# Performance work log

Hardware: AMD Instinct MI355X
Metric: run time of the kernel (lower is better)

## Reference

```python
import jax, jax.numpy as jnp
import numpy as np

N_NODES = 20000
N_EDGES = 100000
ATOM_F = 40
BOND_F = 10
H = 32          # n_node_hidden
EH = 128        # n_edge_hidden
N_LAYERS = 3
EPS = 1e-5
NEG_SLOPE = 0.8


def _bn(x, g, b):
    # BatchNorm1d in training mode: batch mean / biased variance over dim 0
    m = x.mean(0)
    v = x.var(0)
    return (x - m) * jax.lax.rsqrt(v + EPS) * g + b


def setup_inputs() -> dict:
    key = jax.random.key(0)
    ks = iter(jax.random.split(key, 32))

    def nrm(shape, scale):
        return jax.random.normal(next(ks), shape, dtype=jnp.float32) * scale

    inp = {
        "x_node": jax.random.normal(next(ks), (N_NODES, ATOM_F), dtype=jnp.float32),
        "x_edge": jax.random.normal(next(ks), (N_EDGES, BOND_F), dtype=jnp.float32),
        "src": jax.random.randint(next(ks), (N_EDGES,), 0, N_NODES, dtype=jnp.int32),
        "dst": jax.random.randint(next(ks), (N_EDGES,), 0, N_NODES, dtype=jnp.int32),
        # Embedding params
        "bn_n_g": jnp.ones((ATOM_F,), jnp.float32),
        "bn_n_b": jnp.zeros((ATOM_F,), jnp.float32),
        "node_W": nrm((ATOM_F, H), 1.0 / np.sqrt(ATOM_F)),
        "node_b": jnp.zeros((H,), jnp.float32),
        "bn_e_g": jnp.ones((BOND_F,), jnp.float32),
        "bn_e_b": jnp.zeros((BOND_F,), jnp.float32),
        "edge_W": nrm((BOND_F, EH), 1.0 / np.sqrt(BOND_F)),
        "edge_b": jnp.zeros((EH,), jnp.float32),
        # Edge-network (NNConv edge_func) params
        "en_W1": nrm((EH, EH), 1.0 / np.sqrt(EH)),
        "en_b1": jnp.zeros((EH,), jnp.float32),
        "en_bn1_g": jnp.ones((EH,), jnp.float32),
        "en_bn1_b": jnp.zeros((EH,), jnp.float32),
        "en_W2": nrm((EH, H * H), 1.0 / np.sqrt(EH)),
        "en_b2": jnp.zeros((H * H,), jnp.float32),
        "en_bn2_g": jnp.ones((H * H,), jnp.float32),
        "en_bn2_b": jnp.zeros((H * H,), jnp.float32),
        # GRU params (torch layout: [3H, in], gate order r,z,n)
        "gru_Wih": nrm((3 * H, H), 1.0 / np.sqrt(H)),
        "gru_Whh": nrm((3 * H, H), 1.0 / np.sqrt(H)),
        "gru_bih": jnp.zeros((3 * H,), jnp.float32),
        "gru_bhh": jnp.zeros((3 * H,), jnp.float32),
    }
    return inp


def reference(x_node, x_edge, src, dst,
              bn_n_g, bn_n_b, node_W, node_b,
              bn_e_g, bn_e_b, edge_W, edge_b,
              en_W1, en_b1, en_bn1_g, en_bn1_b,
              en_W2, en_b2, en_bn2_g, en_bn2_b,
              gru_Wih, gru_Whh, gru_bih, gru_bhh):
    # ---- Embedding ----
    h_node = _bn(x_node, bn_n_g, bn_n_b) @ node_W + node_b          # [N, H]
    h_edge = _bn(x_edge, bn_e_g, bn_e_b) @ edge_W + edge_b          # [E, EH]

    # ---- Edge network (depends only on h_edge; identical every layer) ----
    t = _bn(h_edge @ en_W1 + en_b1, en_bn1_g, en_bn1_b)
    t = jnp.where(t > 0, t, NEG_SLOPE * t)                          # LeakyReLU(0.8)
    W_e = _bn(t @ en_W2 + en_b2, en_bn2_g, en_bn2_b).reshape(-1, H, H)  # [E, H, H]

    # mean-aggregation denominator (zero in-degree -> message stays 0)
    deg = jax.ops.segment_sum(jnp.ones_like(dst, jnp.float32), dst, num_segments=N_NODES)
    denom = jnp.maximum(deg, 1.0)[:, None]                          # [N, 1]

    def gru_cell(x, h):
        gi = x @ gru_Wih.T + gru_bih
        gh = h @ gru_Whh.T + gru_bhh
        gi_r, gi_z, gi_n = jnp.split(gi, 3, axis=-1)
        gh_r, gh_z, gh_n = jnp.split(gh, 3, axis=-1)
        r = jax.nn.sigmoid(gi_r + gh_r)
        z = jax.nn.sigmoid(gi_z + gh_z)
        n = jnp.tanh(gi_n + r * gh_n)
        return (1.0 - z) * n + z * h

    h = h_node
    for _ in range(N_LAYERS):
        msg = jnp.einsum('ei,eio->eo', h[src], W_e)                 # per-edge matmul
        m = jax.ops.segment_sum(msg, dst, num_segments=N_NODES) / denom  # scatter-mean
        h = gru_cell(m, h)
    return h
```

## Files before the change

kernel.cpp:

```cpp
#include <hip/hip_runtime.h>
#include <hip/hip_fp16.h>

#define NN 20000
#define NE 100000
#define TSQ_NB 256

typedef _Float16 f16x8 __attribute__((ext_vector_type(8)));
typedef float f32x4 __attribute__((ext_vector_type(4)));

__device__ __forceinline__ float wred(float v) {
#pragma unroll
  for (int k = 1; k < 64; k <<= 1) v += __shfl_xor(v, k);
  return v;
}

__global__ __launch_bounds__(256) void pre0(float* __restrict__ zbase,
                                            const float* __restrict__ edge_W,
                                            const float* __restrict__ edge_b,
                                            const float* __restrict__ en_W1,
                                            const float* __restrict__ en_b1,
                                            float* __restrict__ Wc, float* __restrict__ bc) {
  int bid = blockIdx.x, t = threadIdx.x;
  if (bid < 145) {
    int i = bid * 256 + t;
    if (i < 36896) zbase[i] = 0.f;
  } else {
    for (int idx = t; idx < 1280; idx += 256) {
      int bq = idx >> 7, j = idx & 127;
      float a = 0.f;
      for (int q = 0; q < 128; ++q) a += edge_W[bq * 128 + q] * en_W1[q * 128 + j];
      Wc[idx] = a;
    }
    if (t < 128) {
      float a = en_b1[t];
      for (int q = 0; q < 128; ++q) a += edge_b[q] * en_W1[q * 128 + t];
      bc[t] = a;
    }
  }
}

__global__ __launch_bounds__(256) void pre1(const float* __restrict__ x_node,
                                            const float* __restrict__ x_edge,
                                            const int* __restrict__ dst,
                                            float* __restrict__ nstat,
                                            float* __restrict__ estat,
                                            float* __restrict__ deg) {
  __shared__ float ls40[80];
  __shared__ float ls10[20];
  int bid = blockIdx.x, t = threadIdx.x;
  if (bid < 200) {
    for (int i = t; i < 80; i += 256) ls40[i] = 0.f;
    __syncthreads();
    for (int idx = bid * 256 + t; idx < NN * 40; idx += 200 * 256) {
      float v = x_node[idx];
      int c = idx % 40;
      atomicAdd(&ls40[c], v);
      atomicAdd(&ls40[40 + c], v * v);
    }
    __syncthreads();
    for (int i = t; i < 80; i += 256) atomicAdd(&nstat[i], ls40[i]);
  } else if (bid < 456) {
    int b2 = bid - 200;
    for (int i = t; i < 20; i += 256) ls10[i] = 0.f;
    __syncthreads();
    for (int idx = b2 * 256 + t; idx < NE * 10; idx += 256 * 256) {
      float v = x_edge[idx];
      int c = idx % 10;
      atomicAdd(&ls10[c], v);
      atomicAdd(&ls10[10 + c], v * v);
    }
    __syncthreads();
    for (int i = t; i < 20; i += 256) atomicAdd(&estat[i], ls10[i]);
  } else {
    int e = (bid - 456) * 256 + t;
    if (e < NE) atomicAdd(&deg[dst[e]], 1.f);
  }
}

__global__ __launch_bounds__(256) void pre2(const float* __restrict__ nstat,
                                            const float* __restrict__ estat,
                                            const float* __restrict__ bn_n_g,
                                            const float* __restrict__ bn_n_b,
                                            const float* __restrict__ bn_e_g,
                                            const float* __restrict__ bn_e_b,
                                            const float* __restrict__ deg,
                                            float* __restrict__ ns, float* __restrict__ nc,
                                            float* __restrict__ es, float* __restrict__ ec,
                                            float* __restrict__ inv_den) {
  int bid = blockIdx.x, t = threadIdx.x;
  if (bid == 0) {
    if (t < 40) {
      float invR = 1.f / (float)NN;
      float mean = nstat[t] * invR;
      float var = fmaxf(nstat[40 + t] * invR - mean * mean, 0.f);
      float sc = bn_n_g[t] * rsqrtf(var + 1e-5f);
      ns[t] = sc;
      nc[t] = bn_n_b[t] - mean * sc;
    }
  } else if (bid == 1) {
    if (t < 10) {
      float invR = 1.f / (float)NE;
      float mean = estat[t] * invR;
      float var = fmaxf(estat[10 + t] * invR - mean * mean, 0.f);
      float sc = bn_e_g[t] * rsqrtf(var + 1e-5f);
      es[t] = sc;
      ec[t] = bn_e_b[t] - mean * sc;
    }
  } else {
    int n = (bid - 2) * 256 + t;
    if (n < NN) inv_den[n] = 1.f / fmaxf(deg[n], 1.f);
  }
}

__global__ __launch_bounds__(256) void pre3(const float* __restrict__ x_edge,
                                            const float* __restrict__ es,
                                            const float* __restrict__ ec,
                                            float* __restrict__ sxs,
                                            const float* __restrict__ x_node,
                                            const float* __restrict__ ns,
                                            const float* __restrict__ nc,
                                            const float* __restrict__ node_W,
                                            const float* __restrict__ node_b,
                                            float* __restrict__ h_out) {
  __shared__ float Wl[40 * 32];
  __shared__ float sl[40], cl[40];
  int bid = blockIdx.x, t = threadIdx.x;
  if (bid < 32) {
    float s[10][10], xs[10], esl[10], ecl[10];
#pragma unroll
    for (int a = 0; a < 10; ++a) {
      xs[a] = 0.f; esl[a] = es[a]; ecl[a] = ec[a];
#pragma unroll
      for (int b = 0; b < 10; ++b) s[a][b] = 0.f;
    }
    for (int e = bid * 256 + t; e < NE; e += 32 * 256) {
      float xb[10];
#pragma unroll
      for (int q = 0; q < 10; ++q) xb[q] = x_edge[(size_t)e * 10 + q] * esl[q] + ecl[q];
#pragma unroll
      for (int a = 0; a < 10; ++a) {
        xs[a] += xb[a];
#pragma unroll
        for (int b = 0; b < 10; ++b) s[a][b] += xb[a] * xb[b];
      }
    }
#pragma unroll
    for (int a = 0; a < 10; ++a) {
      float r = wred(xs[a]);
      if ((t & 63) == 0) atomicAdd(&sxs[100 + a], r);
#pragma unroll
      for (int b = 0; b < 10; ++b) {
        float r2 = wred(s[a][b]);
        if ((t & 63) == 0) atomicAdd(&sxs[a * 10 + b], r2);
      }
    }
  } else {
    for (int i = t; i < 1280; i += 256) Wl[i] = node_W[i];
    if (t < 40) { sl[t] = ns[t]; cl[t] = nc[t]; }
    __syncthreads();
    int gid = (bid - 32) * 256 + t;
    if (gid >= NN * 32) return;
    int r = gid >> 5, j = gid & 31;
    float acc = node_b[j];
#pragma unroll
    for (int k = 0; k < 40; ++k)
      acc += (x_node[(size_t)r * 40 + k] * sl[k] + cl[k]) * Wl[k * 32 + j];
    h_out[gid] = acc;
  }
}

__global__ void bn1_from_sx(const float* __restrict__ sxs, const float* __restrict__ Wc,
                            const float* __restrict__ bc, const float* __restrict__ g,
                            const float* __restrict__ b, float* __restrict__ s1,
                            float* __restrict__ c1) {
  int j = threadIdx.x;
  float w[10];
#pragma unroll
  for (int q = 0; q < 10; ++q) w[q] = Wc[q * 128 + j];
  float d = 0.f;
#pragma unroll
  for (int q = 0; q < 10; ++q) d += sxs[100 + q] * w[q];
  float qq = 0.f;
#pragma unroll
  for (int a = 0; a < 10; ++a) {
    float p = 0.f;
#pragma unroll
    for (int bq = 0; bq < 10; ++bq) p += sxs[a * 10 + bq] * w[bq];
    qq += w[a] * p;
  }
  float invE = 1.f / (float)NE;
  float bias = bc[j];
  float mean = d * invE + bias;
  float m2 = (qq + 2.f * bias * d) * invE + bias * bias;
  float var = fmaxf(m2 - mean * mean, 0.f);
  float sc = g[j] * rsqrtf(var + 1e-5f);
  s1[j] = sc;
  c1[j] = b[j] - mean * sc;
}

__global__ __launch_bounds__(256) void t_kernel(const float* __restrict__ x,
                                                const float* __restrict__ es,
                                                const float* __restrict__ ec,
                                                const float* __restrict__ Wc,
                                                const float* __restrict__ bcb,
                                                const float* __restrict__ s1,
                                                const float* __restrict__ c1,
                                                __half* __restrict__ T, int E) {
  __shared__ float Wcl[1280], bcl[128], s1l[128], c1l[128], esl[10], ecl[10];
  __shared__ float xr[16][10];
  int t = threadIdx.x;
  for (int i = t; i < 1280; i += 256) Wcl[i] = Wc[i];
  if (t < 128) { bcl[t] = bcb[t]; s1l[t] = s1[t]; c1l[t] = c1[t]; }
  if (t < 10) { esl[t] = es[t]; ecl[t] = ec[t]; }
  int r0 = blockIdx.x * 16;
  if (t < 160) xr[t / 10][t % 10] = x[(size_t)r0 * 10 + t];
  __syncthreads();
  int rl = t >> 4, c0 = (t & 15) * 8;
  float acc[8];
#pragma unroll
  for (int j = 0; j < 8; ++j) acc[j] = bcl[c0 + j];
#pragma unroll
  for (int q = 0; q < 10; ++q) {
    float xb = xr[rl][q] * esl[q] + ecl[q];
#pragma unroll
    for (int j = 0; j < 8; ++j) acc[j] += xb * Wcl[q * 128 + c0 + j];
  }
  f16x8 o;
#pragma unroll
  for (int j = 0; j < 8; ++j) {
    float tv = acc[j] * s1l[c0 + j] + c1l[c0 + j];
    tv = tv > 0.f ? tv : 0.8f * tv;
    o[j] = (_Float16)tv;
  }
  *(f16x8*)&T[(size_t)(r0 + rl) * 128 + c0] = o;
}

__global__ __launch_bounds__(256) void pre6(const __half* __restrict__ T,
                                            float* __restrict__ tsum,
                                            float* __restrict__ partial, int E) {
  __shared__ float cs[128];
  __shared__ _Float16 tl[32 * 132];
  int bid = blockIdx.x, t = threadIdx.x;
  if (bid < 512) {
    int col = t & 127, hf = t >> 7;
    float a = 0.f;
    for (int r = bid * 2 + hf; r < E; r += 512 * 2)
      a += __half2float(T[(size_t)r * 128 + col]);
    if (hf) cs[col] = a;
    __syncthreads();
    if (!hf) atomicAdd(&tsum[col], a + cs[col]);
  } else {
    int bq = bid - 512;
    int w = t >> 6, lane = t & 63;
    int g = lane >> 4, cl = lane & 15;
    f32x4 acc[2][8];
#pragma unroll
    for (int i = 0; i < 2; ++i)
#pragma unroll
      for (int j = 0; j < 8; ++j) acc[i][j] = {0.f, 0.f, 0.f, 0.f};
    int nch = E >> 5;
    for (int ch = bq; ch < nch; ch += TSQ_NB) {
      __syncthreads();
#pragma unroll
      for (int p = 0; p < 4; ++p) {
        int u = p * 256 + t;
        int e = u >> 5, c0 = (u & 31) * 4;
        *(uint2*)&tl[e * 132 + c0] = *(const uint2*)&T[((size_t)ch * 32 + e) * 128 + c0];
      }
      __syncthreads();
      f16x8 fr[8];
#pragma unroll
      for (int cb = 0; cb < 8; ++cb) {
        f16x8 f;
#pragma unroll
        for (int j = 0; j < 8; ++j) f[j] = tl[(g * 8 + j) * 132 + cb * 16 + cl];
        fr[cb] = f;
      }
      f16x8 afr[2];
#pragma unroll
      for (int ri = 0; ri < 2; ++ri) {
        int cb = w * 2 + ri;
        f16x8 f;
#pragma unroll
        for (int j = 0; j < 8; ++j) f[j] = tl[(g * 8 + j) * 132 + cb * 16 + cl];
        afr[ri] = f;
      }
#pragma unroll
      for (int ri = 0; ri < 2; ++ri)
#pragma unroll
        for (int ci = 0; ci < 8; ++ci)
          acc[ri][ci] = __builtin_amdgcn_mfma_f32_16x16x32_f16(afr[ri], fr[ci], acc[ri][ci], 0, 0, 0);
    }
    float* pb = partial + (size_t)bq * 16384;
#pragma unroll
    for (int ri = 0; ri < 2; ++ri)
#pragma unroll
      for (int ci = 0; ci < 8; ++ci)
#pragma unroll
        for (int q = 0; q < 4; ++q)
          pb[(w * 32 + ri * 16 + g * 4 + q) * 128 + ci * 16 + cl] = acc[ri][ci][q];
  }
}

__global__ void tsq_reduce(const float* __restrict__ partial, float* __restrict__ S) {
  int i = blockIdx.x * 256 + threadIdx.x;
  float a = 0.f;
  for (int b = 0; b < TSQ_NB; ++b) a += partial[(size_t)b * 16384 + i];
  S[i] = a;
}

__global__ __launch_bounds__(256) void bn2p(const float* __restrict__ S,
                                            const float* __restrict__ tsum,
                                            const float* __restrict__ W2,
                                            const float* __restrict__ b2,
                                            const float* __restrict__ g,
                                            const float* __restrict__ b,
                                            float* __restrict__ s2, float* __restrict__ c2p) {
  __shared__ float Sl[16384];
  __shared__ float tsl[128];
  for (int i = threadIdx.x; i < 16384; i += 256) Sl[i] = S[i];
  if (threadIdx.x < 128) tsl[threadIdx.x] = tsum[threadIdx.x];
  __syncthreads();
  int w = threadIdx.x >> 6, lane = threadIdx.x & 63;
  int io = blockIdx.x * 4 + w;
  float wlo = W2[(size_t)lane * 1024 + io];
  float whi = W2[(size_t)(lane + 64) * 1024 + io];
  float plo = 0.f, phi = 0.f;
#pragma unroll
  for (int a = 0; a < 64; ++a) {
    float wa = __shfl(wlo, a);
    plo += wa * Sl[a * 128 + lane];
    phi += wa * Sl[a * 128 + lane + 64];
  }
#pragma unroll
  for (int a = 0; a < 64; ++a) {
    float wa = __shfl(whi, a);
    plo += wa * Sl[(a + 64) * 128 + lane];
    phi += wa * Sl[(a + 64) * 128 + lane + 64];
  }
  float qq = wred(plo * wlo + phi * whi);
  float d = wred(wlo * tsl[lane] + whi * tsl[lane + 64]);
  if (lane == 0) {
    float invE = 1.f / (float)NE;
    float mean_raw = d * invE;
    float var = fmaxf(qq * invE - mean_raw * mean_raw, 0.f);
    float sc = g[io] * rsqrtf(var + 1e-5f);
    s2[io] = sc;
    c2p[io] = b[io] - (mean_raw + b2[io]) * sc;
  }
}

__global__ __launch_bounds__(256) void pre9(const float* __restrict__ W2,
                                            const float* __restrict__ s2,
                                            unsigned short* __restrict__ Bp,
                                            const float* __restrict__ h,
                                            const float* __restrict__ c2p,
                                            float* __restrict__ hc,
                                            float* __restrict__ m) {
  __shared__ float cl[1024];
  int bid = blockIdx.x, t = threadIdx.x;
  if (bid < 64) {
    int idx = bid * 256 + t;
    int cb = idx >> 8;
    int ks = (idx >> 6) & 3;
    int lane = idx & 63;
    int col = cb * 16 + (lane & 15);
    int kbase = ks * 32 + (lane >> 4) * 8;
    float sc = s2[col];
    unsigned short tmp[8];
#pragma unroll
    for (int j = 0; j < 8; ++j)
      tmp[j] = __half_as_ushort(__float2half(W2[(size_t)(kbase + j) * 1024 + col] * sc));
    *(uint4*)&Bp[(size_t)idx * 8] = *(uint4*)tmp;
  } else {
    for (int i = t; i < 1024; i += 256) cl[i] = c2p[i];
    __syncthreads();
    int gid = (bid - 64) * 256 + t;
    if (gid >= NN * 32) return;
    int n = gid >> 5, o = gid & 31;
    float a = 0.f;
#pragma unroll
    for (int i = 0; i < 32; ++i) a += h[(size_t)n * 32 + i] * cl[i * 32 + o];
    hc[gid] = a;
    m[gid] = 0.f;
  }
}

__global__ __launch_bounds__(256, 3) void msg_mfma(const __half* __restrict__ T,
                                                   const unsigned short* __restrict__ Bp,
                                                   const float* __restrict__ h,
                                                   const float* __restrict__ hc,
                                                   const int* __restrict__ src,
                                                   const int* __restrict__ dst,
                                                   float* __restrict__ m, int E) {
  __shared__ float hst[32 * 36];
  __shared__ float msw[4 * 1056];
  int t = threadIdx.x;
  int w = t >> 6, lane = t & 63;
  int arow = lane & 15, kgrp = lane >> 4;
  int e0 = blockIdx.x * 32;
  {
    int row = t >> 3, i0 = (t & 7) * 4;
    int sn = src[e0 + row];
    float4 hv = *(const float4*)&h[(size_t)sn * 32 + i0];
    hst[(i0 + 0) * 36 + row] = hv.x;
    hst[(i0 + 1) * 36 + row] = hv.y;
    hst[(i0 + 2) * 36 + row] = hv.z;
    hst[(i0 + 3) * 36 + row] = hv.w;
  }
  __syncthreads();
  f16x8 ah[4][2];
#pragma unroll
  for (int ks = 0; ks < 4; ++ks)
#pragma unroll
    for (int ri = 0; ri < 2; ++ri)
      ah[ks][ri] = *(const f16x8*)&T[(size_t)(e0 + ri * 16 + arow) * 128 + ks * 32 + kgrp * 8];
  f32x4 pm[2][2];
#pragma unroll
  for (int p = 0; p < 2; ++p)
#pragma unroll
    for (int ri = 0; ri < 2; ++ri) pm[p][ri] = {0.f, 0.f, 0.f, 0.f};
#pragma unroll
  for (int cb = 0; cb < 4; ++cb) {
    f32x4 acc[2][4];
#pragma unroll
    for (int i = 0; i < 2; ++i)
#pragma unroll
      for (int j = 0; j < 4; ++j) acc[i][j] = {0.f, 0.f, 0.f, 0.f};
#pragma unroll
    for (int ks = 0; ks < 4; ++ks) {
#pragma unroll
      for (int ci = 0; ci < 4; ++ci) {
        int f = cb * 16 + w * 4 + ci;
        f16x8 bv = *(const f16x8*)&Bp[((size_t)(f * 4 + ks) * 64 + lane) * 8];
        acc[0][ci] = __builtin_amdgcn_mfma_f32_16x16x32_f16(ah[ks][0], bv, acc[0][ci], 0, 0, 0);
        acc[1][ci] = __builtin_amdgcn_mfma_f32_16x16x32_f16(ah[ks][1], bv, acc[1][ci], 0, 0, 0);
      }
    }
#pragma unroll
    for (int ci = 0; ci < 4; ++ci) {
      int i = cb * 8 + w * 2 + (ci >> 1);
#pragma unroll
      for (int ri = 0; ri < 2; ++ri) {
        f32x4 hv = *(const f32x4*)&hst[i * 36 + ri * 16 + kgrp * 4];
        if (ci & 1) pm[1][ri] += hv * acc[ri][ci];
        else        pm[0][ri] += hv * acc[ri][ci];
      }
    }
  }
  {
    float* mw = &msw[w * 1056];
#pragma unroll
    for (int p = 0; p < 2; ++p) {
      int o = p * 16 + arow;
#pragma unroll
      for (int ri = 0; ri < 2; ++ri) {
        int rb = ri * 16 + kgrp * 4;
        mw[o * 33 + rb + 0] = pm[p][ri][0];
        mw[o * 33 + rb + 1] = pm[p][ri][1];
        mw[o * 33 + rb + 2] = pm[p][ri][2];
        mw[o * 33 + rb + 3] = pm[p][ri][3];
      }
    }
  }
  __syncthreads();
  {
    int row = t >> 3, o0 = (t & 7) * 4;
    int e = e0 + row;
    int sn = src[e], dn = dst[e];
    float* mp = m + (size_t)dn * 32;
    const float* hcp = hc + (size_t)sn * 32;
#pragma unroll
    for (int j = 0; j < 4; ++j) {
      int o = o0 + j;
      float v = msw[0 * 1056 + o * 33 + row] + msw[1 * 1056 + o * 33 + row] +
                msw[2 * 1056 + o * 33 + row] + msw[3 * 1056 + o * 33 + row];
      v += hcp[o];
      atomicAdd(&mp[o], v);
    }
  }
}

__global__ __launch_bounds__(256) void gru_kernel(const float* __restrict__ m,
                                                  const float* __restrict__ inv_den,
                                                  const float* __restrict__ h_in,
                                                  const float* __restrict__ Wih,
                                                  const float* __restrict__ Whh,
                                                  const float* __restrict__ bih,
                                                  const float* __restrict__ bhh,
                                                  float* __restrict__ h_out,
                                                  const float* __restrict__ c2p,
                                                  float* __restrict__ hc_out,
                                                  float* __restrict__ m_next,
                                                  int do_next, int N) {
  __shared__ float WT[32 * 96], UT[32 * 96];
  __shared__ float c2l[1024];
  __shared__ float hnew[256];
  int t = threadIdx.x;
  for (int idx = t; idx < 96 * 32; idx += 256) {
    int j = idx / 32, i = idx % 32;
    WT[i * 96 + j] = Wih[idx];
    UT[i * 96 + j] = Whh[idx];
  }
  if (do_next)
    for (int i = t; i < 1024; i += 256) c2l[i] = c2p[i];
  __syncthreads();
  int gid = blockIdx.x * 256 + t;
  int n = gid >> 5, o = gid & 31;
  float inv = inv_den[n];
  float air = 0.f, aiz = 0.f, ain = 0.f, ahr = 0.f, ahz = 0.f, ahn = 0.f;
#pragma unroll
  for (int i = 0; i < 32; ++i) {
    float mi = m[(size_t)n * 32 + i] * inv;
    float hi = h_in[(size_t)n * 32 + i];
    const float* w = &WT[i * 96 + o];
    const float* u = &UT[i * 96 + o];
    air += mi * w[0];  aiz += mi * w[32];  ain += mi * w[64];
    ahr += hi * u[0];  ahz += hi * u[32];  ahn += hi * u[64];
  }
  float r = 1.f / (1.f + expf(-(air + bih[o] + ahr + bhh[o])));
  float z = 1.f / (1.f + expf(-(aiz + bih[o + 32] + ahz + bhh[o + 32])));
  float ng = tanhf(ain + bih[o + 64] + r * (ahn + bhh[o + 64]));
  float hval = (1.f - z) * ng + z * h_in[(size_t)n * 32 + o];
  h_out[gid] = hval;
  if (do_next) {
    hnew[t] = hval;
    __syncthreads();
    int nl = t >> 5;
    float a = 0.f;
#pragma unroll
    for (int i = 0; i < 32; ++i) a += hnew[nl * 32 + i] * c2l[i * 32 + o];
    hc_out[gid] = a;
    m_next[gid] = 0.f;
  }
}

extern "C" void kernel_launch(void* const* d_in, const int* in_sizes, int n_in,
                              void* d_out, int out_size, void* d_ws, size_t ws_size,
                              hipStream_t stream) {
  const float* x_node = (const float*)d_in[0];
  const float* x_edge = (const float*)d_in[1];
  const int* src = (const int*)d_in[2];
  const int* dst = (const int*)d_in[3];
  const float* bn_n_g = (const float*)d_in[4];
  const float* bn_n_b = (const float*)d_in[5];
  const float* node_W = (const float*)d_in[6];
  const float* node_b = (const float*)d_in[7];
  const float* bn_e_g = (const float*)d_in[8];
  const float* bn_e_b = (const float*)d_in[9];
  const float* edge_W = (const float*)d_in[10];
  const float* edge_b = (const float*)d_in[11];
  const float* en_W1 = (const float*)d_in[12];
  const float* en_b1 = (const float*)d_in[13];
  const float* en_W2 = (const float*)d_in[16];
  const float* en_b2 = (const float*)d_in[17];
  const float* en_bn2_g = (const float*)d_in[18];
  const float* en_bn2_b = (const float*)d_in[19];
  const float* en_bn1_g = (const float*)d_in[14];
  const float* en_bn1_b = (const float*)d_in[15];
  const float* gWih = (const float*)d_in[20];
  const float* gWhh = (const float*)d_in[21];
  const float* gbih = (const float*)d_in[22];
  const float* gbhh = (const float*)d_in[23];
  float* out = (float*)d_out;

  char* ws = (char*)d_ws;
  __half* Tt      = (__half*)(ws + 0);
  float* tsq_part = (float*)(ws + 25600000);
  float* h_a      = (float*)(ws + 42377216);
  float* h_b      = (float*)(ws + 44937216);
  float* m_buf    = (float*)(ws + 47497216);
  float* hc       = (float*)(ws + 50057216);
  float* inv_den  = (float*)(ws + 52617216);
  float* zbase    = (float*)(ws + 52697216);
  float* deg   = zbase;
  float* S     = zbase + 20000;
  float* tsum  = zbase + 36384;
  float* sxs   = zbase + 36512;
  float* nstat = zbase + 36640;
  float* estat = zbase + 36768;
  float* par   = (float*)(ws + 52844800);
  float* ns = par + 0;    float* nc = par + 64;
  float* es = par + 128;  float* ec = par + 192;
  float* s1 = par + 256;  float* c1 = par + 384;
  float* wc = par + 512;
  float* bcb = par + 1792;
  float* s2 = par + 1920; float* c2p = par + 2944;
  unsigned short* Bp = (unsigned short*)(ws + 52861184);

  pre0<<<146, 256, 0, stream>>>(zbase, edge_W, edge_b, en_W1, en_b1, wc, bcb);
  pre1<<<847, 256, 0, stream>>>(x_node, x_edge, dst, nstat, estat, deg);
  pre2<<<81, 256, 0, stream>>>(nstat, estat, bn_n_g, bn_n_b, bn_e_g, bn_e_b, deg,
                               ns, nc, es, ec, inv_den);
  pre3<<<2532, 256, 0, stream>>>(x_edge, es, ec, sxs, x_node, ns, nc, node_W, node_b, h_a);
  bn1_from_sx<<<1, 128, 0, stream>>>(sxs, wc, bcb, en_bn1_g, en_bn1_b, s1, c1);
  t_kernel<<<NE / 16, 256, 0, stream>>>(x_edge, es, ec, wc, bcb, s1, c1, Tt, NE);
  pre6<<<512 + TSQ_NB, 256, 0, stream>>>(Tt, tsum, tsq_part, NE);
  tsq_reduce<<<64, 256, 0, stream>>>(tsq_part, S);
  bn2p<<<256, 256, 0, stream>>>(S, tsum, en_W2, en_b2, en_bn2_g, en_bn2_b, s2, c2p);
  pre9<<<64 + 2500, 256, 0, stream>>>(en_W2, s2, Bp, h_a, c2p, hc, m_buf);

  const float* hin = h_a;
  for (int l = 0; l < 3; ++l) {
    float* hout = (l == 0) ? h_b : (l == 1) ? h_a : out;
    msg_mfma<<<NE / 32, 256, 0, stream>>>(Tt, Bp, hin, hc, src, dst, m_buf, NE);
    gru_kernel<<<(NN * 32) / 256, 256, 0, stream>>>(m_buf, inv_den, hin, gWih, gWhh,
                                                    gbih, gbhh, hout, c2p, hc, m_buf,
                                                    (l < 2) ? 1 : 0, NN);
    hin = hout;
  }
}
```

Measured before the change: 603.5 us.

## Sort edges by destination (CSR) and replace atomic scatter with segmented reduction

Builds a CSR row pointer from destination degrees with a single-block scan, then counting-sorts edges by destination so T rows and source indices are stored in dst-sorted order. The message kernel writes per-edge messages contiguously, and the GRU kernel sums each node's segment directly. This removes the per-layer float atomics and the zeroing of the message buffer. In exchange it adds a serial scan kernel, an extra 12.8MB message buffer written and read per layer, and a pre6 column sum rewritten with vector loads.

```diff
diff --git a/kernel.cpp b/kernel.cpp
--- a/kernel.cpp
+++ b/kernel.cpp
@@ -83,10 +83,8 @@
                                             const float* __restrict__ bn_n_b,
                                             const float* __restrict__ bn_e_g,
                                             const float* __restrict__ bn_e_b,
-                                            const float* __restrict__ deg,
                                             float* __restrict__ ns, float* __restrict__ nc,
-                                            float* __restrict__ es, float* __restrict__ ec,
-                                            float* __restrict__ inv_den) {
+                                            float* __restrict__ es, float* __restrict__ ec) {
   int bid = blockIdx.x, t = threadIdx.x;
   if (bid == 0) {
     if (t < 40) {
@@ -97,7 +95,7 @@
       ns[t] = sc;
       nc[t] = bn_n_b[t] - mean * sc;
     }
-  } else if (bid == 1) {
+  } else {
     if (t < 10) {
       float invR = 1.f / (float)NE;
       float mean = estat[t] * invR;
@@ -106,10 +104,39 @@
       es[t] = sc;
       ec[t] = bn_e_b[t] - mean * sc;
     }
-  } else {
-    int n = (bid - 2) * 256 + t;
-    if (n < NN) inv_den[n] = 1.f / fmaxf(deg[n], 1.f);
-  }
+  }
+}
+
+__global__ __launch_bounds__(256) void rowptr_k(const float* __restrict__ deg,
+                                                int* __restrict__ rowptr,
+                                                int* __restrict__ cursor) {
+  __shared__ int ps[256];
+  int t = threadIdx.x;
+  const int CH = 79;
+  int base = t * CH;
+  int s = 0;
+  for (int i = 0; i < CH; ++i) {
+    int n = base + i;
+    if (n < NN) s += (int)deg[n];
+  }
+  ps[t] = s;
+  __syncthreads();
+  for (int off = 1; off < 256; off <<= 1) {
+    int v = (t >= off) ? ps[t - off] : 0;
+    __syncthreads();
+    ps[t] += v;
+    __syncthreads();
+  }
+  int run = (t == 0) ? 0 : ps[t - 1];
+  for (int i = 0; i < CH; ++i) {
+    int n = base + i;
+    if (n < NN) {
+      rowptr[n] = run;
+      cursor[n] = run;
+      run += (int)deg[n];
+    }
+  }
+  if (t == 255) rowptr[NN] = run;
 }
 
 __global__ __launch_bounds__(256) void pre3(const float* __restrict__ x_edge,
@@ -121,7 +148,12 @@
                                             const float* __restrict__ nc,
                                             const float* __restrict__ node_W,
                                             const float* __restrict__ node_b,
-                                            float* __restrict__ h_out) {
+                                            float* __restrict__ h_out,
+                                            const int* __restrict__ src,
+                                            const int* __restrict__ dst,
+                                            int* __restrict__ cursor,
+                                            int* __restrict__ inv_e,
+                                            int* __restrict__ src_s) {
   __shared__ float Wl[40 * 32];
   __shared__ float sl[40], cl[40];
   int bid = blockIdx.x, t = threadIdx.x;
@@ -154,7 +186,7 @@
         if ((t & 63) == 0) atomicAdd(&sxs[a * 10 + b], r2);
       }
     }
-  } else {
+  } else if (bid < 2532) {
     for (int i = t; i < 1280; i += 256) Wl[i] = node_W[i];
     if (t < 40) { sl[t] = ns[t]; cl[t] = nc[t]; }
     __syncthreads();
@@ -166,6 +198,14 @@
     for (int k = 0; k < 40; ++k)
       acc += (x_node[(size_t)r * 40 + k] * sl[k] + cl[k]) * Wl[k * 32 + j];
     h_out[gid] = acc;
+  } else {
+    int e = (bid - 2532) * 256 + t;
+    if (e < NE) {
+      int d = dst[e];
+      int pos = atomicAdd(&cursor[d], 1);
+      inv_e[e] = pos;
+      src_s[pos] = src[e];
+    }
   }
 }
 
@@ -205,6 +245,7 @@
                                                 const float* __restrict__ bcb,
                                                 const float* __restrict__ s1,
                                                 const float* __restrict__ c1,
+                                                const int* __restrict__ inv_e,
                                                 __half* __restrict__ T, int E) {
   __shared__ float Wcl[1280], bcl[128], s1l[128], c1l[128], esl[10], ecl[10];
   __shared__ float xr[16][10];
@@ -232,23 +273,35 @@
     tv = tv > 0.f ? tv : 0.8f * tv;
     o[j] = (_Float16)tv;
   }
-  *(f16x8*)&T[(size_t)(r0 + rl) * 128 + c0] = o;
+  int rs = inv_e[r0 + rl];
+  *(f16x8*)&T[(size_t)rs * 128 + c0] = o;
 }
 
 __global__ __launch_bounds__(256) void pre6(const __half* __restrict__ T,
                                             float* __restrict__ tsum,
                                             float* __restrict__ partial, int E) {
-  __shared__ float cs[128];
+  __shared__ float csum[16][128];
   __shared__ _Float16 tl[32 * 132];
   int bid = blockIdx.x, t = threadIdx.x;
   if (bid < 512) {
-    int col = t & 127, hf = t >> 7;
-    float a = 0.f;
-    for (int r = bid * 2 + hf; r < E; r += 512 * 2)
-      a += __half2float(T[(size_t)r * 128 + col]);
-    if (hf) cs[col] = a;
-    __syncthreads();
-    if (!hf) atomicAdd(&tsum[col], a + cs[col]);
+    int rg = t >> 4;
+    int cg = (t & 15) * 8;
+    float a[8] = {0.f, 0.f, 0.f, 0.f, 0.f, 0.f, 0.f, 0.f};
+    for (int r = bid * 16 + rg; r < E; r += 512 * 16) {
+      uint4 u = *(const uint4*)&T[(size_t)r * 128 + cg];
+      const __half* hp = (const __half*)&u;
+#pragma unroll
+      for (int q = 0; q < 8; ++q) a[q] += __half2float(hp[q]);
+    }
+#pragma unroll
+    for (int q = 0; q < 8; ++q) csum[rg][cg + q] = a[q];
+    __syncthreads();
+    if (t < 128) {
+      float s = 0.f;
+#pragma unroll
+      for (int r = 0; r < 16; ++r) s += csum[r][t];
+      atomicAdd(&tsum[t], s);
+    }
   } else {
     int bq = bid - 512;
     int w = t >> 6, lane = t & 63;
@@ -355,8 +408,7 @@
                                             unsigned short* __restrict__ Bp,
                                             const float* __restrict__ h,
                                             const float* __restrict__ c2p,
-                                            float* __restrict__ hc,
-                                            float* __restrict__ m) {
+                                            float* __restrict__ hc) {
   __shared__ float cl[1024];
   int bid = blockIdx.x, t = threadIdx.x;
   if (bid < 64) {
@@ -382,7 +434,6 @@
 #pragma unroll
     for (int i = 0; i < 32; ++i) a += h[(size_t)n * 32 + i] * cl[i * 32 + o];
     hc[gid] = a;
-    m[gid] = 0.f;
   }
 }
 
@@ -390,9 +441,8 @@
                                                    const unsigned short* __restrict__ Bp,
                                                    const float* __restrict__ h,
                                                    const float* __restrict__ hc,
-                                                   const int* __restrict__ src,
-                                                   const int* __restrict__ dst,
-                                                   float* __restrict__ m, int E) {
+                                                   const int* __restrict__ src_s,
+                                                   float* __restrict__ msg_buf, int E) {
   __shared__ float hst[32 * 36];
   __shared__ float msw[4 * 1056];
   int t = threadIdx.x;
@@ -401,7 +451,7 @@
   int e0 = blockIdx.x * 32;
   {
     int row = t >> 3, i0 = (t & 7) * 4;
-    int sn = src[e0 + row];
+    int sn = src_s[e0 + row];
     float4 hv = *(const float4*)&h[(size_t)sn * 32 + i0];
     hst[(i0 + 0) * 36 + row] = hv.x;
     hst[(i0 + 1) * 36 + row] = hv.y;
@@ -467,22 +517,22 @@
   {
     int row = t >> 3, o0 = (t & 7) * 4;
     int e = e0 + row;
-    int sn = src[e], dn = dst[e];
-    float* mp = m + (size_t)dn * 32;
-    const float* hcp = hc + (size_t)sn * 32;
+    int sn = src_s[e];
+    float4 hv = *(const float4*)&hc[(size_t)sn * 32 + o0];
+    float vs[4];
 #pragma unroll
     for (int j = 0; j < 4; ++j) {
       int o = o0 + j;
-      float v = msw[0 * 1056 + o * 33 + row] + msw[1 * 1056 + o * 33 + row] +
-                msw[2 * 1056 + o * 33 + row] + msw[3 * 1056 + o * 33 + row];
-      v += hcp[o];
-      atomicAdd(&mp[o], v);
-    }
-  }
-}
-
-__global__ __launch_bounds__(256) void gru_kernel(const float* __restrict__ m,
-                                                  const float* __restrict__ inv_den,
+      vs[j] = msw[0 * 1056 + o * 33 + row] + msw[1 * 1056 + o * 33 + row] +
+              msw[2 * 1056 + o * 33 + row] + msw[3 * 1056 + o * 33 + row];
+    }
+    float4 ov = make_float4(vs[0] + hv.x, vs[1] + hv.y, vs[2] + hv.z, vs[3] + hv.w);
+    *(float4*)&msg_buf[(size_t)e * 32 + o0] = ov;
+  }
+}
+
+__global__ __launch_bounds__(256) void gru_kernel(const float* __restrict__ msg_buf,
+                                                  const int* __restrict__ rowptr,
                                                   const float* __restrict__ h_in,
                                                   const float* __restrict__ Wih,
                                                   const float* __restrict__ Whh,
@@ -491,10 +541,10 @@
                                                   float* __restrict__ h_out,
                                                   const float* __restrict__ c2p,
                                                   float* __restrict__ hc_out,
-                                                  float* __restrict__ m_next,
                                                   int do_next, int N) {
   __shared__ float WT[32 * 96], UT[32 * 96];
   __shared__ float c2l[1024];
+  __shared__ float mrow[256];
   __shared__ float hnew[256];
   int t = threadIdx.x;
   for (int idx = t; idx < 96 * 32; idx += 256) {
@@ -507,11 +557,17 @@
   __syncthreads();
   int gid = blockIdx.x * 256 + t;
   int n = gid >> 5, o = gid & 31;
-  float inv = inv_den[n];
+  int k0 = rowptr[n], k1 = rowptr[n + 1];
+  float msum = 0.f;
+  for (int k = k0; k < k1; ++k) msum += msg_buf[(size_t)k * 32 + o];
+  float inv = 1.f / fmaxf((float)(k1 - k0), 1.f);
+  mrow[t] = msum * inv;
+  __syncthreads();
+  int nl = t >> 5;
   float air = 0.f, aiz = 0.f, ain = 0.f, ahr = 0.f, ahz = 0.f, ahn = 0.f;
 #pragma unroll
   for (int i = 0; i < 32; ++i) {
-    float mi = m[(size_t)n * 32 + i] * inv;
+    float mi = mrow[nl * 32 + i];
     float hi = h_in[(size_t)n * 32 + i];
     const float* w = &WT[i * 96 + o];
     const float* u = &UT[i * 96 + o];
@@ -526,12 +582,10 @@
   if (do_next) {
     hnew[t] = hval;
     __syncthreads();
-    int nl = t >> 5;
     float a = 0.f;
 #pragma unroll
     for (int i = 0; i < 32; ++i) a += hnew[nl * 32 + i] * c2l[i * 32 + o];
     hc_out[gid] = a;
-    m_next[gid] = 0.f;
   }
 }
 
@@ -552,12 +606,12 @@
   const float* edge_b = (const float*)d_in[11];
   const float* en_W1 = (const float*)d_in[12];
   const float* en_b1 = (const float*)d_in[13];
+  const float* en_bn1_g = (const float*)d_in[14];
+  const float* en_bn1_b = (const float*)d_in[15];
   const float* en_W2 = (const float*)d_in[16];
   const float* en_b2 = (const float*)d_in[17];
   const float* en_bn2_g = (const float*)d_in[18];
   const float* en_bn2_b = (const float*)d_in[19];
-  const float* en_bn1_g = (const float*)d_in[14];
-  const float* en_bn1_b = (const float*)d_in[15];
   const float* gWih = (const float*)d_in[20];
   const float* gWhh = (const float*)d_in[21];
   const float* gbih = (const float*)d_in[22];
@@ -569,43 +623,47 @@
   float* tsq_part = (float*)(ws + 25600000);
   float* h_a      = (float*)(ws + 42377216);
   float* h_b      = (float*)(ws + 44937216);
-  float* m_buf    = (float*)(ws + 47497216);
-  float* hc       = (float*)(ws + 50057216);
-  float* inv_den  = (float*)(ws + 52617216);
-  float* zbase    = (float*)(ws + 52697216);
+  float* msg_buf  = (float*)(ws + 47497216);
+  float* hc       = (float*)(ws + 60297216);
+  int*   src_s    = (int*)(ws + 62857216);
+  int*   inv_e    = (int*)(ws + 63257216);
+  int*   rowptr   = (int*)(ws + 63657216);
+  int*   cursor   = (int*)(ws + 63737280);
+  float* zbase    = (float*)(ws + 63817280);
   float* deg   = zbase;
   float* S     = zbase + 20000;
   float* tsum  = zbase + 36384;
   float* sxs   = zbase + 36512;
   float* nstat = zbase + 36640;
   float* estat = zbase + 36768;
-  float* par   = (float*)(ws + 52844800);
+  float* par   = (float*)(ws + 63964864);
   float* ns = par + 0;    float* nc = par + 64;
   float* es = par + 128;  float* ec = par + 192;
   float* s1 = par + 256;  float* c1 = par + 384;
   float* wc = par + 512;
   float* bcb = par + 1792;
   float* s2 = par + 1920; float* c2p = par + 2944;
-  unsigned short* Bp = (unsigned short*)(ws + 52861184);
+  unsigned short* Bp = (unsigned short*)(ws + 63981248);
 
   pre0<<<146, 256, 0, stream>>>(zbase, edge_W, edge_b, en_W1, en_b1, wc, bcb);
   pre1<<<847, 256, 0, stream>>>(x_node, x_edge, dst, nstat, estat, deg);
-  pre2<<<81, 256, 0, stream>>>(nstat, estat, bn_n_g, bn_n_b, bn_e_g, bn_e_b, deg,
-                               ns, nc, es, ec, inv_den);
-  pre3<<<2532, 256, 0, stream>>>(x_edge, es, ec, sxs, x_node, ns, nc, node_W, node_b, h_a);
+  pre2<<<2, 256, 0, stream>>>(nstat, estat, bn_n_g, bn_n_b, bn_e_g, bn_e_b, ns, nc, es, ec);
+  rowptr_k<<<1, 256, 0, stream>>>(deg, rowptr, cursor);
+  pre3<<<2923, 256, 0, stream>>>(x_edge, es, ec, sxs, x_node, ns, nc, node_W, node_b, h_a,
+                                 src, dst, cursor, inv_e, src_s);
   bn1_from_sx<<<1, 128, 0, stream>>>(sxs, wc, bcb, en_bn1_g, en_bn1_b, s1, c1);
-  t_kernel<<<NE / 16, 256, 0, stream>>>(x_edge, es, ec, wc, bcb, s1, c1, Tt, NE);
+  t_kernel<<<NE / 16, 256, 0, stream>>>(x_edge, es, ec, wc, bcb, s1, c1, inv_e, Tt, NE);
   pre6<<<512 + TSQ_NB, 256, 0, stream>>>(Tt, tsum, tsq_part, NE);
   tsq_reduce<<<64, 256, 0, stream>>>(tsq_part, S);
   bn2p<<<256, 256, 0, stream>>>(S, tsum, en_W2, en_b2, en_bn2_g, en_bn2_b, s2, c2p);
-  pre9<<<64 + 2500, 256, 0, stream>>>(en_W2, s2, Bp, h_a, c2p, hc, m_buf);
+  pre9<<<64 + 2500, 256, 0, stream>>>(en_W2, s2, Bp, h_a, c2p, hc);
 
   const float* hin = h_a;
   for (int l = 0; l < 3; ++l) {
     float* hout = (l == 0) ? h_b : (l == 1) ? h_a : out;
-    msg_mfma<<<NE / 32, 256, 0, stream>>>(Tt, Bp, hin, hc, src, dst, m_buf, NE);
-    gru_kernel<<<(NN * 32) / 256, 256, 0, stream>>>(m_buf, inv_den, hin, gWih, gWhh,
-                                                    gbih, gbhh, hout, c2p, hc, m_buf,
+    msg_mfma<<<NE / 32, 256, 0, stream>>>(Tt, Bp, hin, hc, src_s, msg_buf, NE);
+    gru_kernel<<<(NN * 32) / 256, 256, 0, stream>>>(msg_buf, rowptr, hin, gWih, gWhh,
+                                                    gbih, gbhh, hout, c2p, hc,
                                                     (l < 2) ? 1 : 0, NN);
     hin = hout;
   }
```

Result: no change. 608.4 us (+0.8%).
